# Kernel optimization log

Measured on AMD Instinct MI355X. Metric: run time of the kernel, lower is better.

Reference implementation:

```python
import jax, jax.numpy as jnp
import numpy as np

BETA = 0.25  # commitment loss weight (standard VQ-VAE beta)


def setup_inputs() -> dict:
    key = jax.random.key(0)
    k1, k2 = jax.random.split(key)
    N, D, Q, K = 131072, 128, 4, 1024
    x = jax.random.normal(k1, (N, D), dtype=jnp.float32)
    codebooks = jax.random.normal(k2, (Q, K, D), dtype=jnp.float32)
    return {"x": x, "codebooks": codebooks}


def reference(x, codebooks):
    """Residual VQ: sequentially quantize the residual against each codebook.

    x:         [N, D] float
    codebooks: [Q, K, D] float (one [K, D] codebook per quantizer stage)
    Returns (x_q [N, D], mean_loss scalar, indices [N, Q] int32).
    """
    sg = jax.lax.stop_gradient

    def stage(carry, E):
        residual, x_q = carry                      # [N, D], [N, D]
        # squared euclidean distances: ||r||^2 - 2 r.E^T + ||E||^2  -> [N, K]
        d = (jnp.sum(residual * residual, axis=1, keepdims=True)
             - 2.0 * (residual @ E.T)
             + jnp.sum(E * E, axis=1))
        idx = jnp.argmin(d, axis=1)                # [N]
        q = E[idx]                                 # [N, D] gather
        # codebook loss + beta * commitment loss
        loss = (jnp.mean((q - sg(residual)) ** 2)
                + BETA * jnp.mean((sg(q) - residual) ** 2))
        # straight-through estimator
        q_st = residual + sg(q - residual)
        return (residual - q_st, x_q + q_st), (loss, idx)

    (_, x_q), (losses, idxs) = jax.lax.scan(
        stage, (x, jnp.zeros_like(x)), codebooks)
    mean_loss = jnp.mean(losses)
    all_indices = jnp.transpose(idxs)              # [Q, N] -> [N, Q], stacked dim=-1
    return x_q, mean_loss, all_indices
```

## Files before the change

kernel.cpp:

```cpp
#include <hip/hip_runtime.h>

#define N_ROWS 131072
#define DIM    128
#define QST    4
#define KC     1024
#define BM     256
#define NTH    512
#define PNTH   256
#define NWAVE  8
#define NCHUNK 32
#define EPS    6e-3f
#define FLAGB  (1 << 16)

typedef _Float16 h8  __attribute__((ext_vector_type(8)));
typedef float    fx4 __attribute__((ext_vector_type(4)));

typedef __attribute__((address_space(3))) void lds_void;
typedef const __attribute__((address_space(1))) void glb_void;

#define MFMA16(a, b, c) __builtin_amdgcn_mfma_f32_16x16x32_f16((a), (b), (c), 0, 0, 0)

__global__ void k_prep(const float* __restrict__ cb,
                       double* __restrict__ cvec64, float* __restrict__ cvec32,
                       _Float16* __restrict__ packB) {
  int gid = blockIdx.x * blockDim.x + threadIdx.x;
  if (gid >= QST * KC) return;
  int q = gid >> 10, code = gid & (KC - 1);
  int ch = code >> 5, ctl = (code >> 4) & 1, n = code & 15;
  const float* e = cb + ((size_t)q * KC + code) * DIM;
  double s = 0.0;
  for (int d = 0; d < DIM; d++) {
    float v = e[d];
    s = fma((double)v, (double)v, s);
    int kt = d >> 5, g = (d >> 3) & 3, j = d & 7;
    int lane = g * 16 + n;
    size_t base = ((size_t)q * NCHUNK + ch) * 8192
                + (size_t)((ctl * 4 + kt) * 2) * 512 + lane * 8 + j;
    _Float16 hh = (_Float16)v;
    packB[base]       = hh;
    packB[base + 512] = (_Float16)(v - (float)hh);
  }
  cvec64[q * KC + code] = s;
  cvec32[q * KC + code] = (float)s;
}

__global__ __launch_bounds__(NTH, 4) void k_stage(
    int st, const float* rin, float* rout, const float* __restrict__ x,
    const float* __restrict__ cb,
    const double* __restrict__ cvec64, const float* __restrict__ cvec32,
    const _Float16* __restrict__ packB,
    float* __restrict__ oidx, float* __restrict__ lpart, int final_stage)
{
  extern __shared__ float smem[];
  _Float16* Bl      = (_Float16*)smem;
  float*    cvecL   = smem + 16384;
  int*      idxs    = (int*)(smem + 17408);
  double*   redd    = (double*)(smem + 17664);
  int*      redi    = (int*)(smem + 17680);
  float*    redf    = smem + 17688;
  int*      flags   = (int*)(smem + 17696);

  const int tid = threadIdx.x;
  const int lane = tid & 63, wv = tid >> 6;
  const int tx = tid & 15;
  const size_t rowbase = (size_t)blockIdx.x * BM;

  const double*   cq64 = cvec64 + st * KC;
  const float*    cq32 = cvec32 + st * KC;
  const float*    Eq   = cb + (size_t)st * KC * DIM;
  const _Float16* PBq  = packB + (size_t)st * 262144;

  for (int i = tid; i < KC; i += NTH) cvecL[i] = cq32[i];

  h8 ah[2][4], al[2][4];
  #pragma unroll
  for (int rt = 0; rt < 2; rt++) {
    const float* rowp = rin + (rowbase + wv * 32 + rt * 16 + (lane & 15)) * (size_t)DIM
                        + ((lane >> 4) * 8);
    #pragma unroll
    for (int kt = 0; kt < 4; kt++) {
      float4 f0 = *(const float4*)(rowp + kt * 32);
      float4 f1 = *(const float4*)(rowp + kt * 32 + 4);
      float vv[8] = {f0.x, f0.y, f0.z, f0.w, f1.x, f1.y, f1.z, f1.w};
      #pragma unroll
      for (int j = 0; j < 8; j++) {
        _Float16 hh = (_Float16)vv[j];
        ah[rt][kt][j] = hh;
        al[rt][kt][j] = (_Float16)(vv[j] - (float)hh);
      }
    }
  }

  asm volatile("s_waitcnt vmcnt(0) lgkmcnt(0)" ::: "memory");

  auto stageB = [&](int ch, int buf) {
    const _Float16* src = PBq + (size_t)ch * 8192 + wv * 1024 + lane * 8;
    _Float16* dst = Bl + buf * 8192 + wv * 1024;
    #pragma unroll
    for (int i = 0; i < 2; i++)
      __builtin_amdgcn_global_load_lds((glb_void*)(src + i * 512),
                                       (lds_void*)(dst + i * 512), 16, 0, 0);
  };

  float b1[8], b2[8];
  int   i1[8];
  #pragma unroll
  for (int i = 0; i < 8; i++) { b1[i] = 3.4e38f; b2[i] = 3.4e38f; i1[i] = 0; }

  const fx4 zero4 = {0.f, 0.f, 0.f, 0.f};

  stageB(0, 0); stageB(1, 1); stageB(2, 2);

  #pragma unroll 1
  for (int ch = 0; ch < NCHUNK; ch++) {
    if (ch < NCHUNK - 2)       asm volatile("s_waitcnt vmcnt(4)" ::: "memory");
    else if (ch == NCHUNK - 2) asm volatile("s_waitcnt vmcnt(2)" ::: "memory");
    else                       asm volatile("s_waitcnt vmcnt(0)" ::: "memory");
    __builtin_amdgcn_s_barrier();
    asm volatile("" ::: "memory");
    if (ch + 3 < NCHUNK) stageB(ch + 3, (ch + 3) & 3);

    const _Float16* Bb = Bl + (ch & 3) * 8192;
    fx4 acc[2][2];
    acc[0][0] = zero4; acc[0][1] = zero4; acc[1][0] = zero4; acc[1][1] = zero4;

    __builtin_amdgcn_s_setprio(1);
    #pragma unroll
    for (int kt = 0; kt < 4; kt++) {
      #pragma unroll
      for (int ct = 0; ct < 2; ct++) {
        const _Float16* p = Bb + (size_t)((ct * 4 + kt) * 2) * 512 + lane * 8;
        h8 bh = *(const h8*)p;
        h8 bl = *(const h8*)(p + 512);
        acc[0][ct] = MFMA16(ah[0][kt], bh, acc[0][ct]);
        acc[1][ct] = MFMA16(ah[1][kt], bh, acc[1][ct]);
        acc[0][ct] = MFMA16(al[0][kt], bh, acc[0][ct]);
        acc[1][ct] = MFMA16(al[1][kt], bh, acc[1][ct]);
        acc[0][ct] = MFMA16(ah[0][kt], bl, acc[0][ct]);
        acc[1][ct] = MFMA16(ah[1][kt], bl, acc[1][ct]);
      }
    }
    __builtin_amdgcn_s_setprio(0);

    #pragma unroll
    for (int ct = 0; ct < 2; ct++) {
      int code = ch * 32 + ct * 16 + tx;
      float cvv = cvecL[code];
      #pragma unroll
      for (int rt = 0; rt < 2; rt++) {
        #pragma unroll
        for (int j = 0; j < 4; j++) {
          float sc = fmaf(-2.f, acc[rt][ct][j], cvv);
          int r = rt * 4 + j;
          if (sc < b1[r]) { b2[r] = b1[r]; b1[r] = sc; i1[r] = code; }
          else            { b2[r] = fminf(b2[r], sc); }
        }
      }
    }
  }

  #pragma unroll
  for (int m = 1; m < 16; m <<= 1) {
    #pragma unroll
    for (int r = 0; r < 8; r++) {
      float ob1 = __shfl_xor(b1[r], m, 64);
      int   oi1 = __shfl_xor(i1[r], m, 64);
      float ob2 = __shfl_xor(b2[r], m, 64);
      bool take = (ob1 < b1[r]) || (ob1 == b1[r] && oi1 < i1[r]);
      float loser = take ? b1[r] : ob1;
      if (take) { b1[r] = ob1; i1[r] = oi1; }
      b2[r] = fminf(fminf(b2[r], ob2), loser);
    }
  }

  if (tx == 0) {
    int g = lane >> 4;
    #pragma unroll
    for (int rt = 0; rt < 2; rt++)
      #pragma unroll
      for (int j = 0; j < 4; j++) {
        int r = rt * 4 + j;
        int fl = (b2[r] - b1[r] <= EPS) ? FLAGB : 0;
        idxs[wv * 32 + rt * 16 + g * 4 + j] = i1[r] | fl;
      }
  }
  __syncthreads();

  {
    bool pred = (tid < BM) && (idxs[tid] & FLAGB);
    unsigned long long bal = __ballot(pred);
    if (lane == 0) flags[wv] = (bal != 0ull) ? 1 : 0;
  }
  __syncthreads();
  int anyflag = flags[0] | flags[1] | flags[2] | flags[3]
              | flags[4] | flags[5] | flags[6] | flags[7];
  if (anyflag) {
    for (int row = 0; row < BM; row++) {
      if (!(idxs[row] & FLAGB)) continue;
      const float* rrow = rin + (rowbase + row) * (size_t)DIM;
      double dot[2] = {0.0, 0.0};
      for (int d = 0; d < DIM; d++) {
        double a = (double)rrow[d];
        #pragma unroll
        for (int c = 0; c < 2; c++)
          dot[c] = fma(a, (double)Eq[(size_t)(tid + c * NTH) * DIM + d], dot[c]);
      }
      double bs = 1e300; int bk = 0;
      #pragma unroll
      for (int c = 0; c < 2; c++) {
        int k = tid + c * NTH;
        double s = fma(-2.0, dot[c], cq64[k]);
        if (s < bs || (s == bs && k < bk)) { bs = s; bk = k; }
      }
      #pragma unroll
      for (int m = 1; m < 64; m <<= 1) {
        double ob = __shfl_xor(bs, m, 64);
        int    ok = __shfl_xor(bk, m, 64);
        if (ob < bs || (ob == bs && ok < bk)) { bs = ob; bk = ok; }
      }
      if (lane == 0) { redd[wv] = bs; redi[wv] = bk; }
      __syncthreads();
      if (tid == 0) {
        double fb = redd[0]; int fk = redi[0];
        #pragma unroll
        for (int w = 1; w < NWAVE; w++) {
          if (redd[w] < fb || (redd[w] == fb && redi[w] < fk)) { fb = redd[w]; fk = redi[w]; }
        }
        idxs[row] = fk;
      }
      __syncthreads();
    }
  }

  {
    float lsum = 0.f;
    #pragma unroll 1
    for (int it = 0; it < 16; it++) {
      int g = it * NTH + tid;
      int row = g >> 5, c4 = g & 31;
      int kidx = idxs[row] & 1023;
      if ((g & 31) == 0) oidx[(rowbase + row) * 4 + st] = (float)kidx;
      float4 ev = *(const float4*)(Eq + (size_t)kidx * DIM + c4 * 4);
      float4 rv = *(const float4*)(rin + (rowbase + row) * (size_t)DIM + c4 * 4);
      float4 dv = make_float4(rv.x - ev.x, rv.y - ev.y, rv.z - ev.z, rv.w - ev.w);
      lsum = fmaf(dv.x, dv.x, lsum);
      lsum = fmaf(dv.y, dv.y, lsum);
      lsum = fmaf(dv.z, dv.z, lsum);
      lsum = fmaf(dv.w, dv.w, lsum);
      float4 wv4 = dv;
      if (final_stage) {
        float4 xv = *(const float4*)(x + (rowbase + row) * (size_t)DIM + c4 * 4);
        wv4 = make_float4(xv.x - dv.x, xv.y - dv.y, xv.z - dv.z, xv.w - dv.w);
      }
      *(float4*)(rout + (rowbase + row) * (size_t)DIM + c4 * 4) = wv4;
    }
    #pragma unroll
    for (int m = 1; m < 64; m <<= 1) lsum += __shfl_xor(lsum, m, 64);
    if (lane == 0) redf[wv] = lsum;
    __syncthreads();
    if (tid == 0) {
      float t = 0.f;
      #pragma unroll
      for (int w = 0; w < NWAVE; w++) t += redf[w];
      lpart[st * (N_ROWS / BM) + blockIdx.x] = t;
    }
  }
}

__global__ void k_loss(const float* __restrict__ part, float* __restrict__ o) {
  __shared__ float red[4];
  int tid = threadIdx.x;
  float s = 0.f;
  for (int i = tid; i < QST * (N_ROWS / BM); i += PNTH) s += part[i];
  #pragma unroll
  for (int m = 1; m < 64; m <<= 1) s += __shfl_xor(s, m, 64);
  if ((tid & 63) == 0) red[tid >> 6] = s;
  __syncthreads();
  if (tid == 0)
    o[0] = (red[0] + red[1] + red[2] + red[3]) *
           (1.25f / ((float)QST * (float)N_ROWS * (float)DIM));
}

extern "C" void kernel_launch(void* const* d_in, const int* in_sizes, int n_in,
                              void* d_out, int out_size, void* d_ws, size_t ws_size,
                              hipStream_t stream) {
  const float* x  = (const float*)d_in[0];
  const float* cb = (const float*)d_in[1];
  float* out = (float*)d_out;
  float* ws  = (float*)d_ws;

  float*    r      = out;
  double*   cvec64 = (double*)ws;
  float*    cvec32 = (float*)(cvec64 + (size_t)QST * KC);
  float*    part   = cvec32 + (size_t)QST * KC;
  _Float16* packB  = (_Float16*)(part + (size_t)QST * (N_ROWS / BM));

  float* out_loss = out + (size_t)N_ROWS * DIM;
  float* out_idx  = out_loss + 1;

  static const size_t SMEM = 17704 * sizeof(float);
  hipFuncSetAttribute(reinterpret_cast<const void*>(k_stage),
                      hipFuncAttributeMaxDynamicSharedMemorySize, (int)SMEM);

  k_prep<<<(QST * KC + PNTH - 1) / PNTH, PNTH, 0, stream>>>(cb, cvec64, cvec32, packB);

  for (int s = 0; s < QST; s++) {
    const float* rin = (s == 0) ? x : r;
    k_stage<<<N_ROWS / BM, NTH, SMEM, stream>>>(s, rin, r, x, cb, cvec64, cvec32,
                                                packB, out_idx, part,
                                                (s == QST - 1) ? 1 : 0);
  }

  k_loss<<<1, PNTH, 0, stream>>>(part, out_loss);
}
```

Before: 675.4 us.

## Shrink stage blocks to 128 rows and 16-code chunks with triple buffering

Halves the row tile per block (256 threads, 4 waves) and halves the codebook chunk to 16 codes, repacking the fp16 split codebook layout to match. The LDS pipeline drops from a 4-buffer, 3-ahead prefetch to a 3-buffer, 2-ahead ring, and shared memory shrinks from about 70KB to 29KB so more blocks can fit per CU. The fallback fp64 rescoring now loops over 4 codes per thread. In exchange, each wave issues half as many MFMAs per barrier, so synchronization overhead per unit of work roughly doubles, and each codebook chunk is reused across fewer rows.

After: 652.3 us. 3.4% less time.

```diff
diff --git a/kernel.cpp b/kernel.cpp
--- a/kernel.cpp
+++ b/kernel.cpp
@@ -4,11 +4,11 @@
 #define DIM    128
 #define QST    4
 #define KC     1024
-#define BM     256
-#define NTH    512
+#define BM     128
+#define NTH    256
 #define PNTH   256
-#define NWAVE  8
-#define NCHUNK 32
+#define NWAVE  4
+#define NCHUNK 64
 #define EPS    6e-3f
 #define FLAGB  (1 << 16)
 
@@ -26,7 +26,7 @@
   int gid = blockIdx.x * blockDim.x + threadIdx.x;
   if (gid >= QST * KC) return;
   int q = gid >> 10, code = gid & (KC - 1);
-  int ch = code >> 5, ctl = (code >> 4) & 1, n = code & 15;
+  int ch = code >> 4, n = code & 15;
   const float* e = cb + ((size_t)q * KC + code) * DIM;
   double s = 0.0;
   for (int d = 0; d < DIM; d++) {
@@ -34,8 +34,7 @@
     s = fma((double)v, (double)v, s);
     int kt = d >> 5, g = (d >> 3) & 3, j = d & 7;
     int lane = g * 16 + n;
-    size_t base = ((size_t)q * NCHUNK + ch) * 8192
-                + (size_t)((ctl * 4 + kt) * 2) * 512 + lane * 8 + j;
+    size_t base = ((size_t)q * NCHUNK + ch) * 4096 + (size_t)kt * 1024 + lane * 8 + j;
     _Float16 hh = (_Float16)v;
     packB[base]       = hh;
     packB[base + 512] = (_Float16)(v - (float)hh);
@@ -53,12 +52,12 @@
 {
   extern __shared__ float smem[];
   _Float16* Bl      = (_Float16*)smem;
-  float*    cvecL   = smem + 16384;
-  int*      idxs    = (int*)(smem + 17408);
-  double*   redd    = (double*)(smem + 17664);
-  int*      redi    = (int*)(smem + 17680);
-  float*    redf    = smem + 17688;
-  int*      flags   = (int*)(smem + 17696);
+  float*    cvecL   = smem + 6144;
+  int*      idxs    = (int*)(smem + 7168);
+  double*   redd    = (double*)(smem + 7296);
+  int*      redi    = (int*)(smem + 7304);
+  float*    redf    = smem + 7308;
+  int*      flags   = (int*)(smem + 7312);
 
   const int tid = threadIdx.x;
   const int lane = tid & 63, wv = tid >> 6;
@@ -92,10 +91,11 @@
   }
 
   asm volatile("s_waitcnt vmcnt(0) lgkmcnt(0)" ::: "memory");
+  __syncthreads();
 
   auto stageB = [&](int ch, int buf) {
-    const _Float16* src = PBq + (size_t)ch * 8192 + wv * 1024 + lane * 8;
-    _Float16* dst = Bl + buf * 8192 + wv * 1024;
+    const _Float16* src = PBq + (size_t)ch * 4096 + wv * 1024 + lane * 8;
+    _Float16* dst = Bl + buf * 4096 + wv * 1024;
     #pragma unroll
     for (int i = 0; i < 2; i++)
       __builtin_amdgcn_global_load_lds((glb_void*)(src + i * 512),
@@ -109,54 +109,52 @@
 
   const fx4 zero4 = {0.f, 0.f, 0.f, 0.f};
 
-  stageB(0, 0); stageB(1, 1); stageB(2, 2);
-
+  stageB(0, 0); stageB(1, 1);
+
+  int buf = 0, bufStage = 2;
   #pragma unroll 1
   for (int ch = 0; ch < NCHUNK; ch++) {
-    if (ch < NCHUNK - 2)       asm volatile("s_waitcnt vmcnt(4)" ::: "memory");
-    else if (ch == NCHUNK - 2) asm volatile("s_waitcnt vmcnt(2)" ::: "memory");
-    else                       asm volatile("s_waitcnt vmcnt(0)" ::: "memory");
+    if (ch < NCHUNK - 1) asm volatile("s_waitcnt vmcnt(2)" ::: "memory");
+    else                 asm volatile("s_waitcnt vmcnt(0)" ::: "memory");
     __builtin_amdgcn_s_barrier();
     asm volatile("" ::: "memory");
-    if (ch + 3 < NCHUNK) stageB(ch + 3, (ch + 3) & 3);
-
-    const _Float16* Bb = Bl + (ch & 3) * 8192;
-    fx4 acc[2][2];
-    acc[0][0] = zero4; acc[0][1] = zero4; acc[1][0] = zero4; acc[1][1] = zero4;
+    if (ch + 2 < NCHUNK) stageB(ch + 2, bufStage);
+
+    const _Float16* Bb = Bl + buf * 4096;
+    fx4 acc[2];
+    acc[0] = zero4; acc[1] = zero4;
 
     __builtin_amdgcn_s_setprio(1);
     #pragma unroll
     for (int kt = 0; kt < 4; kt++) {
-      #pragma unroll
-      for (int ct = 0; ct < 2; ct++) {
-        const _Float16* p = Bb + (size_t)((ct * 4 + kt) * 2) * 512 + lane * 8;
-        h8 bh = *(const h8*)p;
-        h8 bl = *(const h8*)(p + 512);
-        acc[0][ct] = MFMA16(ah[0][kt], bh, acc[0][ct]);
-        acc[1][ct] = MFMA16(ah[1][kt], bh, acc[1][ct]);
-        acc[0][ct] = MFMA16(al[0][kt], bh, acc[0][ct]);
-        acc[1][ct] = MFMA16(al[1][kt], bh, acc[1][ct]);
-        acc[0][ct] = MFMA16(ah[0][kt], bl, acc[0][ct]);
-        acc[1][ct] = MFMA16(ah[1][kt], bl, acc[1][ct]);
-      }
+      const _Float16* p = Bb + (size_t)kt * 1024 + lane * 8;
+      h8 bh = *(const h8*)p;
+      h8 bl = *(const h8*)(p + 512);
+      acc[0] = MFMA16(ah[0][kt], bh, acc[0]);
+      acc[1] = MFMA16(ah[1][kt], bh, acc[1]);
+      acc[0] = MFMA16(al[0][kt], bh, acc[0]);
+      acc[1] = MFMA16(al[1][kt], bh, acc[1]);
+      acc[0] = MFMA16(ah[0][kt], bl, acc[0]);
+      acc[1] = MFMA16(ah[1][kt], bl, acc[1]);
     }
     __builtin_amdgcn_s_setprio(0);
 
-    #pragma unroll
-    for (int ct = 0; ct < 2; ct++) {
-      int code = ch * 32 + ct * 16 + tx;
+    {
+      int code = ch * 16 + tx;
       float cvv = cvecL[code];
       #pragma unroll
       for (int rt = 0; rt < 2; rt++) {
         #pragma unroll
         for (int j = 0; j < 4; j++) {
-          float sc = fmaf(-2.f, acc[rt][ct][j], cvv);
+          float sc = fmaf(-2.f, acc[rt][j], cvv);
           int r = rt * 4 + j;
           if (sc < b1[r]) { b2[r] = b1[r]; b1[r] = sc; i1[r] = code; }
           else            { b2[r] = fminf(b2[r], sc); }
         }
       }
     }
+    buf = (buf == 2) ? 0 : buf + 1;
+    bufStage = (bufStage == 2) ? 0 : bufStage + 1;
   }
 
   #pragma unroll
@@ -192,22 +190,21 @@
     if (lane == 0) flags[wv] = (bal != 0ull) ? 1 : 0;
   }
   __syncthreads();
-  int anyflag = flags[0] | flags[1] | flags[2] | flags[3]
-              | flags[4] | flags[5] | flags[6] | flags[7];
+  int anyflag = flags[0] | flags[1] | flags[2] | flags[3];
   if (anyflag) {
     for (int row = 0; row < BM; row++) {
       if (!(idxs[row] & FLAGB)) continue;
       const float* rrow = rin + (rowbase + row) * (size_t)DIM;
-      double dot[2] = {0.0, 0.0};
+      double dot[4] = {0.0, 0.0, 0.0, 0.0};
       for (int d = 0; d < DIM; d++) {
         double a = (double)rrow[d];
         #pragma unroll
-        for (int c = 0; c < 2; c++)
+        for (int c = 0; c < 4; c++)
           dot[c] = fma(a, (double)Eq[(size_t)(tid + c * NTH) * DIM + d], dot[c]);
       }
       double bs = 1e300; int bk = 0;
       #pragma unroll
-      for (int c = 0; c < 2; c++) {
+      for (int c = 0; c < 4; c++) {
         int k = tid + c * NTH;
         double s = fma(-2.0, dot[c], cq64[k]);
         if (s < bs || (s == bs && k < bk)) { bs = s; bk = k; }
@@ -298,7 +295,7 @@
   float* out_loss = out + (size_t)N_ROWS * DIM;
   float* out_idx  = out_loss + 1;
 
-  static const size_t SMEM = 17704 * sizeof(float);
+  static const size_t SMEM = 7316 * sizeof(float);
   hipFuncSetAttribute(reinterpret_cast<const void*>(k_stage),
                       hipFuncAttributeMaxDynamicSharedMemorySize, (int)SMEM);
 
```
